# Kernel optimization log

Measured on AMD Instinct MI355X. Metric: run time of the kernel, lower is better.

Reference implementation:

```python
import jax, jax.numpy as jnp
import numpy as np

NA = 3        # anchors per scale
NC = 80       # classes
NO = NC + 5   # outputs per anchor
STRIDES = (8.0, 16.0, 32.0)


def setup_inputs() -> dict:
    key = jax.random.key(0)
    ks = jax.random.split(key, 10)
    inp = {
        "p0": jax.random.normal(ks[0], (16, 256, 80, 80), jnp.float32),
        "p1": jax.random.normal(ks[1], (16, 512, 40, 40), jnp.float32),
        "p2": jax.random.normal(ks[2], (16, 1024, 20, 20), jnp.float32),
        "w0": jax.random.normal(ks[3], (255, 256), jnp.float32) * 0.02,
        "b0": jax.random.normal(ks[4], (255,), jnp.float32) * 0.02,
        "w1": jax.random.normal(ks[5], (255, 512), jnp.float32) * 0.02,
        "b1": jax.random.normal(ks[6], (255,), jnp.float32) * 0.02,
        "w2": jax.random.normal(ks[7], (255, 1024), jnp.float32) * 0.02,
        "b2": jax.random.normal(ks[8], (255,), jnp.float32) * 0.02,
        # YOLOv5 default anchors (pixel units), shape [nl, na, 2]
        "anchors": jnp.asarray(np.array(
            [[[10, 13], [16, 30], [33, 23]],
             [[30, 61], [62, 45], [59, 119]],
             [[116, 90], [156, 198], [373, 326]]], dtype=np.float32)),
    }
    return inp


def _decode_scale(p, w, b, anc, stride):
    # p: [bs, C, ny, nx]; w: [na*no, C]; anc: [na, 2] pixel anchors
    bs, _, ny, nx = p.shape
    y = jnp.einsum('bchw,oc->bohw', p, w) + b[None, :, None, None]   # 1x1 conv
    y = y.reshape(bs, NA, NO, ny, nx).transpose(0, 1, 3, 4, 2)       # [bs,na,ny,nx,no]
    s = jax.nn.sigmoid(y)
    gy, gx = jnp.meshgrid(jnp.arange(ny, dtype=p.dtype),
                          jnp.arange(nx, dtype=p.dtype), indexing='ij')
    grid = jnp.stack((gx, gy), axis=-1)[None, None] - 0.5            # [1,1,ny,nx,2]
    xy = (s[..., :2] * 2 + grid) * stride
    wh = (s[..., 2:4] * 2) ** 2 * anc.reshape(1, NA, 1, 1, 2)
    out = jnp.concatenate((xy, wh, s[..., 4:]), axis=-1)
    return out.reshape(bs, NA * ny * nx, NO)


def reference(p0, p1, p2, w0, b0, w1, b1, w2, b2, anchors):
    feats = (p0, p1, p2)
    ws = (w0, w1, w2)
    bs_ = (b0, b1, b2)
    z = [_decode_scale(feats[i], ws[i], bs_[i], anchors[i], STRIDES[i])
         for i in range(3)]
    return jnp.concatenate(z, axis=1)  # [bs, sum(na*ny*nx), no]
```

## Files before the change

### kernel.cpp

```cpp
#include <hip/hip_runtime.h>
#include <math.h>


#define NOUT 85
#define TOTAL_ROWS 25200

typedef __attribute__((ext_vector_type(8))) short short8;
typedef __attribute__((ext_vector_type(4))) float floatx4;

__device__ __forceinline__ unsigned short f2bf(float x) {
    union { float f; unsigned u; } v; v.f = x;
    unsigned r = v.u + 0x7fffu + ((v.u >> 16) & 1u);
    return (unsigned short)(r >> 16);
}

__global__ __launch_bounds__(256) void convert_w_all(
    const float* __restrict__ w0, const float* __restrict__ w1,
    const float* __restrict__ w2, unsigned short* __restrict__ dst)
{
    int i = blockIdx.x * 256 + threadIdx.x;
    const float* w; int C, idx;
    if (i < 65536)       { w = w0; C = 256;  idx = i; }
    else if (i < 196608) { w = w1; C = 512;  idx = i - 65536; }
    else                 { w = w2; C = 1024; idx = i - 196608; }
    int m = idx / C, c = idx - m * C;
    float v = (m < 255) ? w[(size_t)m * C + c] : 0.f;
    dst[i] = f2bf(v);
}

__global__ __launch_bounds__(256) void yolo_fused(
    const float* __restrict__ p0, const float* __restrict__ p1,
    const float* __restrict__ p2, const unsigned short* __restrict__ wsA,
    const float* __restrict__ b0v, const float* __restrict__ b1v,
    const float* __restrict__ b2v, const float* __restrict__ anc,
    float* __restrict__ out)
{
    __shared__ __align__(16) unsigned short Bl[2][64 * 32];

    const int tid = threadIdx.x;
    const int l   = tid & 63;
    const int wv  = tid >> 6;
    const int ml  = l & 15;
    const int q   = l >> 4;

    const int x = blockIdx.x;
    const float* p; const unsigned short* wA; const float* bias; const float* an;
    int C, HW, row_off, sh, tile, b; float stride_;
    if (x < 112) {
        b = x / 7;  tile = x - b * 7;
        p = p2; wA = wsA + 196608; bias = b2v; an = anc + 12;
        C = 1024; HW = 400; row_off = 24000; sh = 2; stride_ = 32.f;
    } else if (x < 512) {
        int i = x - 112; b = i / 25; tile = i - b * 25;
        p = p1; wA = wsA + 65536; bias = b1v; an = anc + 6;
        C = 512; HW = 1600; row_off = 19200; sh = 3; stride_ = 16.f;
    } else {
        int i = x - 512; b = i / 100; tile = i - b * 100;
        p = p0; wA = wsA; bias = b0v; an = anc;
        C = 256; HW = 6400; row_off = 0; sh = 4; stride_ = 8.f;
    }
    const int hw0   = tile * 64;
    const int iters = C >> 5;

    floatx4 acc[4][4];
#pragma unroll
    for (int ni = 0; ni < 4; ++ni)
#pragma unroll
        for (int mi = 0; mi < 4; ++mi)
            acc[ni][mi] = floatx4{0.f, 0.f, 0.f, 0.f};

    const float* pb = p + (size_t)b * C * HW;
    int scol = hw0 + l; if (scol >= HW) scol = HW - 1;
    const float* pcur = pb + (size_t)(wv * 8) * HW + scol;
    const size_t kjump = (size_t)32 * HW;

    const int wchunk = wv ^ (l & 3) ^ ((l >> 2) & 3);
    const unsigned short* wbase = wA + (size_t)(wv * 64 + ml) * C + q * 8;

    float bv[8];
#pragma unroll
    for (int r = 0; r < 8; ++r) bv[r] = pcur[(size_t)r * HW];
    pcur += kjump;
    {
        unsigned pk0 = (unsigned)f2bf(bv[0]) | ((unsigned)f2bf(bv[1]) << 16);
        unsigned pk1 = (unsigned)f2bf(bv[2]) | ((unsigned)f2bf(bv[3]) << 16);
        unsigned pk2 = (unsigned)f2bf(bv[4]) | ((unsigned)f2bf(bv[5]) << 16);
        unsigned pk3 = (unsigned)f2bf(bv[6]) | ((unsigned)f2bf(bv[7]) << 16);
        ((uint4*)Bl[0])[l * 4 + wchunk] = make_uint4(pk0, pk1, pk2, pk3);
    }
#pragma unroll
    for (int r = 0; r < 8; ++r) bv[r] = pcur[(size_t)r * HW];
    pcur += kjump;
    asm volatile("s_waitcnt lgkmcnt(0)" ::: "memory");
    __builtin_amdgcn_s_barrier();
    asm volatile("" ::: "memory");

    for (int it = 0; it < iters; ++it) {
        const unsigned short* Bc = Bl[it & 1];
        short8 wf[4];
#pragma unroll
        for (int mi = 0; mi < 4; ++mi)
            wf[mi] = *(const short8*)(wbase + (size_t)(mi * 16) * C + it * 32);
        short8 pf[4];
#pragma unroll
        for (int ni = 0; ni < 4; ++ni) {
            int n  = ni * 16 + ml;
            int ck = q ^ (n & 3) ^ ((n >> 2) & 3);
            pf[ni] = *(const short8*)(Bc + n * 32 + ck * 8);
        }
        if (it + 1 < iters) {
            unsigned pk0 = (unsigned)f2bf(bv[0]) | ((unsigned)f2bf(bv[1]) << 16);
            unsigned pk1 = (unsigned)f2bf(bv[2]) | ((unsigned)f2bf(bv[3]) << 16);
            unsigned pk2 = (unsigned)f2bf(bv[4]) | ((unsigned)f2bf(bv[5]) << 16);
            unsigned pk3 = (unsigned)f2bf(bv[6]) | ((unsigned)f2bf(bv[7]) << 16);
            ((uint4*)Bl[(it & 1) ^ 1])[l * 4 + wchunk] = make_uint4(pk0, pk1, pk2, pk3);
            if (it + 2 < iters) {
#pragma unroll
                for (int r = 0; r < 8; ++r) bv[r] = pcur[(size_t)r * HW];
                pcur += kjump;
            }
        }
        asm volatile("s_waitcnt lgkmcnt(0)" ::: "memory");
        __builtin_amdgcn_s_barrier();
        asm volatile("" ::: "memory");
#pragma unroll
        for (int ni = 0; ni < 4; ++ni)
#pragma unroll
            for (int mi = 0; mi < 4; ++mi)
                acc[ni][mi] = __builtin_amdgcn_mfma_f32_16x16x32_bf16(
                    pf[ni], wf[mi], acc[ni][mi], 0, 0, 0);
    }

    const int nx = 5 << sh;
#pragma unroll
    for (int mi = 0; mi < 4; ++mi) {
        const int  o     = wv * 64 + mi * 16 + ml;
        const bool valid = (o < 255);
        const int  osafe = valid ? o : 254;
        const int  a     = osafe / 85;
        const int  oo    = osafe - a * 85;
        const float bi   = bias[osafe];
        const float anw  = an[a * 2 + 0];
        const float anh  = an[a * 2 + 1];
        float* orow = out + ((size_t)b * TOTAL_ROWS + row_off + a * HW) * NOUT + oo;
#pragma unroll
        for (int ni = 0; ni < 4; ++ni) {
            const int hwb = hw0 + ni * 16 + q * 4;
            if (hwb >= HW) continue;
#pragma unroll
            for (int r = 0; r < 4; ++r) {
                const int hw = hwb + r;
                float y = acc[ni][mi][r] + bi;
                float s = 1.f / (1.f + __expf(-y));
                float v;
                if (oo >= 4) {
                    v = s;
                } else {
                    unsigned gy = (unsigned)(((unsigned long long)(unsigned)(hw >> sh)
                                             * 0xCCCCCCCDull) >> 34);
                    int gx = hw - (int)gy * nx;
                    if (oo == 0)      v = (2.f * s + (float)gx - 0.5f) * stride_;
                    else if (oo == 1) v = (2.f * s + (float)gy - 0.5f) * stride_;
                    else { float t = 2.f * s; v = t * t * ((oo == 2) ? anw : anh); }
                }
                if (valid) orow[(size_t)hw * NOUT] = v;
            }
        }
    }
}

extern "C" void kernel_launch(void* const* d_in, const int* in_sizes, int n_in,
                              void* d_out, int out_size, void* d_ws, size_t ws_size,
                              hipStream_t stream) {
    const float* p0 = (const float*)d_in[0];
    const float* p1 = (const float*)d_in[1];
    const float* p2 = (const float*)d_in[2];
    const float* w0 = (const float*)d_in[3];
    const float* b0 = (const float*)d_in[4];
    const float* w1 = (const float*)d_in[5];
    const float* b1 = (const float*)d_in[6];
    const float* w2 = (const float*)d_in[7];
    const float* b2 = (const float*)d_in[8];
    const float* anc = (const float*)d_in[9];
    float* out = (float*)d_out;

    unsigned short* wsA = (unsigned short*)d_ws;

    convert_w_all<<<dim3(458752 / 256), dim3(256), 0, stream>>>(w0, w1, w2, wsA);

    yolo_fused<<<dim3(2112), dim3(256), 0, stream>>>(
        p0, p1, p2, wsA, b0, b1, b2, anc, out);
}
```

Before: 351.2 us.

## Pre-swizzle bf16 weights into MFMA fragment order and deepen activation prefetch

The weight conversion kernel now writes bf16 weights already arranged in MFMA fragment order, so each lane loads its 16-byte fragment with coalesced contiguous reads instead of strided row reads. The main loop is unrolled by two with separate ping-pong buffers and register sets, prefetching activations two K-steps ahead and loading weights one step ahead of use. The aim is to hide global memory latency behind MFMA work. The cost is higher register pressure, which may reduce occupancy.

```diff
diff --git a/kernel.cpp b/kernel.cpp
--- a/kernel.cpp
+++ b/kernel.cpp
@@ -23,8 +23,13 @@
     if (i < 65536)       { w = w0; C = 256;  idx = i; }
     else if (i < 196608) { w = w1; C = 512;  idx = i - 65536; }
     else                 { w = w2; C = 1024; idx = i - 196608; }
-    int m = idx / C, c = idx - m * C;
-    float v = (m < 255) ? w[(size_t)m * C + c] : 0.f;
+    int j  = idx & 7;
+    int l  = (idx >> 3) & 63;
+    int t  = idx >> 9;
+    int ot = t & 15, kt = t >> 4;
+    int o  = ot * 16 + (l & 15);
+    int k  = kt * 32 + (l >> 4) * 8 + j;
+    float v = (o < 255) ? w[(size_t)o * C + k] : 0.f;
     dst[i] = f2bf(v);
 }
 
@@ -35,7 +40,8 @@
     const float* __restrict__ b2v, const float* __restrict__ anc,
     float* __restrict__ out)
 {
-    __shared__ __align__(16) unsigned short Bl[2][64 * 32];
+    __shared__ __align__(16) unsigned short Bl0[64 * 32];
+    __shared__ __align__(16) unsigned short Bl1[64 * 32];
 
     const int tid = threadIdx.x;
     const int l   = tid & 63;
@@ -71,64 +77,62 @@
 
     const float* pb = p + (size_t)b * C * HW;
     int scol = hw0 + l; if (scol >= HW) scol = HW - 1;
-    const float* pcur = pb + (size_t)(wv * 8) * HW + scol;
-    const size_t kjump = (size_t)32 * HW;
+    const float* pcol0 = pb + (size_t)(wv * 8) * HW + scol;
+    const size_t kj = (size_t)32 * HW;
 
     const int wchunk = wv ^ (l & 3) ^ ((l >> 2) & 3);
-    const unsigned short* wbase = wA + (size_t)(wv * 64 + ml) * C + q * 8;
-
-    float bv[8];
-#pragma unroll
-    for (int r = 0; r < 8; ++r) bv[r] = pcur[(size_t)r * HW];
-    pcur += kjump;
-    {
-        unsigned pk0 = (unsigned)f2bf(bv[0]) | ((unsigned)f2bf(bv[1]) << 16);
-        unsigned pk1 = (unsigned)f2bf(bv[2]) | ((unsigned)f2bf(bv[3]) << 16);
-        unsigned pk2 = (unsigned)f2bf(bv[4]) | ((unsigned)f2bf(bv[5]) << 16);
-        unsigned pk3 = (unsigned)f2bf(bv[6]) | ((unsigned)f2bf(bv[7]) << 16);
-        ((uint4*)Bl[0])[l * 4 + wchunk] = make_uint4(pk0, pk1, pk2, pk3);
-    }
-#pragma unroll
-    for (int r = 0; r < 8; ++r) bv[r] = pcur[(size_t)r * HW];
-    pcur += kjump;
-    asm volatile("s_waitcnt lgkmcnt(0)" ::: "memory");
-    __builtin_amdgcn_s_barrier();
-    asm volatile("" ::: "memory");
-
-    for (int it = 0; it < iters; ++it) {
-        const unsigned short* Bc = Bl[it & 1];
-        short8 wf[4];
-#pragma unroll
-        for (int mi = 0; mi < 4; ++mi)
-            wf[mi] = *(const short8*)(wbase + (size_t)(mi * 16) * C + it * 32);
-        short8 pf[4];
-#pragma unroll
-        for (int ni = 0; ni < 4; ++ni) {
-            int n  = ni * 16 + ml;
-            int ck = q ^ (n & 3) ^ ((n >> 2) & 3);
-            pf[ni] = *(const short8*)(Bc + n * 32 + ck * 8);
+    const unsigned short* wfb = wA + ((size_t)(wv * 4) << 9) + (l << 3);
+
+    float  bvA[8], bvB[8];
+    short8 wfA[4], wfB[4];
+
+#define LOADBV(dst, s) do { const float* _pc = pcol0 + (size_t)(s) * kj;          \
+        _Pragma("unroll") for (int _r = 0; _r < 8; ++_r)                          \
+            dst[_r] = _pc[(size_t)_r * HW]; } while (0)
+#define LOADWF(dst, s) do { const unsigned short* _wb = wfb + (size_t)(s) * 8192; \
+        _Pragma("unroll") for (int _m = 0; _m < 4; ++_m)                          \
+            dst[_m] = *(const short8*)(_wb + (_m << 9)); } while (0)
+#define PACK(src, BUF) do {                                                       \
+        unsigned _p0 = (unsigned)f2bf(src[0]) | ((unsigned)f2bf(src[1]) << 16);   \
+        unsigned _p1 = (unsigned)f2bf(src[2]) | ((unsigned)f2bf(src[3]) << 16);   \
+        unsigned _p2 = (unsigned)f2bf(src[4]) | ((unsigned)f2bf(src[5]) << 16);   \
+        unsigned _p3 = (unsigned)f2bf(src[6]) | ((unsigned)f2bf(src[7]) << 16);   \
+        ((uint4*)BUF)[l * 4 + wchunk] = make_uint4(_p0, _p1, _p2, _p3); } while (0)
+#define READPF(pf, BUF) do { _Pragma("unroll") for (int _n = 0; _n < 4; ++_n) {   \
+        int _nn = _n * 16 + ml; int _ck = q ^ (_nn & 3) ^ ((_nn >> 2) & 3);       \
+        pf[_n] = *(const short8*)(BUF + _nn * 32 + _ck * 8); } } while (0)
+#define MFMA16(pf, wf) do { _Pragma("unroll") for (int _n = 0; _n < 4; ++_n)      \
+        _Pragma("unroll") for (int _m = 0; _m < 4; ++_m)                          \
+            acc[_n][_m] = __builtin_amdgcn_mfma_f32_16x16x32_bf16(                \
+                pf[_n], wf[_m], acc[_n][_m], 0, 0, 0); } while (0)
+#define LGKM_BARRIER() do { asm volatile("s_waitcnt lgkmcnt(0)" ::: "memory");    \
+        __builtin_amdgcn_s_barrier(); asm volatile("" ::: "memory"); } while (0)
+
+    LOADBV(bvA, 0);
+    LOADBV(bvB, 1);
+    LOADWF(wfA, 0);
+    PACK(bvA, Bl0);
+    LOADBV(bvA, 2);
+    LGKM_BARRIER();
+
+    for (int it = 0; it < iters; it += 2) {
+        short8 pfA[4];
+        READPF(pfA, Bl0);
+        PACK(bvB, Bl1);
+        if (it + 3 < iters) LOADBV(bvB, it + 3);
+        LOADWF(wfB, it + 1);
+        LGKM_BARRIER();
+        MFMA16(pfA, wfA);
+
+        short8 pfB[4];
+        READPF(pfB, Bl1);
+        if (it + 2 < iters) {
+            PACK(bvA, Bl0);
+            if (it + 4 < iters) LOADBV(bvA, it + 4);
+            LOADWF(wfA, it + 2);
+            LGKM_BARRIER();
         }
-        if (it + 1 < iters) {
-            unsigned pk0 = (unsigned)f2bf(bv[0]) | ((unsigned)f2bf(bv[1]) << 16);
-            unsigned pk1 = (unsigned)f2bf(bv[2]) | ((unsigned)f2bf(bv[3]) << 16);
-            unsigned pk2 = (unsigned)f2bf(bv[4]) | ((unsigned)f2bf(bv[5]) << 16);
-            unsigned pk3 = (unsigned)f2bf(bv[6]) | ((unsigned)f2bf(bv[7]) << 16);
-            ((uint4*)Bl[(it & 1) ^ 1])[l * 4 + wchunk] = make_uint4(pk0, pk1, pk2, pk3);
-            if (it + 2 < iters) {
-#pragma unroll
-                for (int r = 0; r < 8; ++r) bv[r] = pcur[(size_t)r * HW];
-                pcur += kjump;
-            }
-        }
-        asm volatile("s_waitcnt lgkmcnt(0)" ::: "memory");
-        __builtin_amdgcn_s_barrier();
-        asm volatile("" ::: "memory");
-#pragma unroll
-        for (int ni = 0; ni < 4; ++ni)
-#pragma unroll
-            for (int mi = 0; mi < 4; ++mi)
-                acc[ni][mi] = __builtin_amdgcn_mfma_f32_16x16x32_bf16(
-                    pf[ni], wf[mi], acc[ni][mi], 0, 0, 0);
+        MFMA16(pfB, wfB);
     }
 
     const int nx = 5 << sh;
@@ -167,6 +171,12 @@
             }
         }
     }
+#undef LOADBV
+#undef LOADWF
+#undef PACK
+#undef READPF
+#undef MFMA16
+#undef LGKM_BARRIER
 }
 
 extern "C" void kernel_launch(void* const* d_in, const int* in_sizes, int n_in,
```

New measurement: 339.9 us. 1.03x faster.
